# Performance work log

Hardware: AMD Instinct MI355X
Metric: run time of the kernel (lower is better)

The kernel has to match this reference:

```python
import jax, jax.numpy as jnp
import numpy as np

NQ = 4  # n_qubits_per_head


def _apply_ry(state, theta, q):
    # state: (N, 2,2,2,2) real amplitudes; theta: (N,) per-element angle; wire q
    st = jnp.moveaxis(state, 1 + q, -1)
    c = jnp.cos(0.5 * theta).reshape(-1, 1, 1, 1)
    s = jnp.sin(0.5 * theta).reshape(-1, 1, 1, 1)
    a0, a1 = st[..., 0], st[..., 1]
    st = jnp.stack([c * a0 - s * a1, s * a0 + c * a1], axis=-1)
    return jnp.moveaxis(st, -1, 1 + q)


def _apply_cnot(state, ctrl, tgt):
    st = jnp.moveaxis(state, (1 + ctrl, 1 + tgt), (-2, -1))
    st = jnp.stack([st[..., 0, :], st[..., 1, ::-1]], axis=-2)
    return jnp.moveaxis(st, (-2, -1), (1 + ctrl, 1 + tgt))


def _quantum_circuit(x_in, par):
    # x_in: (N, NQ) data angles; par: (N, L, NQ) variational angles (per head, tiled)
    N = x_in.shape[0]
    L = par.shape[1]
    state = jnp.zeros((N, 2, 2, 2, 2), x_in.dtype).at[:, 0, 0, 0, 0].set(1.0)
    for l in range(L):
        for q in range(NQ):
            state = _apply_ry(state, par[:, l, q], q)
        for q in range(NQ - 1):
            state = _apply_cnot(state, q, q + 1)
        state = _apply_cnot(state, NQ - 1, 0)
    for q in range(NQ):
        state = _apply_ry(state, x_in[:, q], q)
    p = state * state  # probabilities (real amplitudes: only RY/CNOT gates)
    zs = []
    for q in range(NQ):
        st = jnp.moveaxis(p, 1 + q, -1)
        zs.append(jnp.sum(st[..., 0], axis=(1, 2, 3)) - jnp.sum(st[..., 1], axis=(1, 2, 3)))
    return jnp.stack(zs, axis=-1)  # (N, NQ)


def setup_inputs() -> dict:
    key = jax.random.key(0)
    ks = jax.random.split(key, 6)
    B, T, E, H, L = 4, 2048, 1024, 16, 2
    scale = 1.0 / np.sqrt(E)
    x = jax.random.normal(ks[0], (B, T, E), dtype=jnp.float32)
    Wq = jax.random.normal(ks[1], (E, E), dtype=jnp.float32) * scale
    Wk = jax.random.normal(ks[2], (E, E), dtype=jnp.float32) * scale
    Wv = jax.random.normal(ks[3], (E, E), dtype=jnp.float32) * scale
    Wo = jax.random.normal(ks[4], (E, E), dtype=jnp.float32) * scale
    qparams = jax.random.normal(ks[5], (H, L, NQ), dtype=jnp.float32)
    return {"x": x, "Wq": Wq, "Wk": Wk, "Wv": Wv, "Wo": Wo, "qparams": qparams}


def reference(x, Wq, Wk, Wv, Wo, qparams):
    B, T, E = x.shape
    H, L, _ = qparams.shape
    hd = E // H
    q = x @ Wq.T
    k = x @ Wk.T
    v = x @ Wv.T
    # NOTE: original scales by sqrt(embed_dim), not sqrt(head_dim)
    scores = jnp.einsum('bte,bse->bts', q, k) / jnp.sqrt(jnp.asarray(E, x.dtype))
    w = jax.nn.softmax(scores, axis=-1)
    out = jnp.einsum('bts,bse->bte', w, v)
    oh = out.reshape(B, T, H, hd)
    N = B * T * H
    xin = oh[..., :NQ].reshape(N, NQ)
    par = jnp.broadcast_to(qparams[None, None], (B, T, H, L, NQ)).reshape(N, L, NQ)
    z = _quantum_circuit(xin, par)  # (N, NQ)
    zfull = jnp.concatenate([z, jnp.zeros((N, hd - NQ), x.dtype)], axis=-1)
    return zfull.reshape(B, T, E) @ Wo.T
```

## Files before the change

### kernel.cpp

```cpp
#include <hip/hip_runtime.h>
#include <hip/hip_fp16.h>

typedef _Float16 half_t;
typedef __attribute__((ext_vector_type(4))) _Float16 half4;
typedef __attribute__((ext_vector_type(8))) _Float16 half8;
typedef __attribute__((ext_vector_type(4))) float floatx4;

__device__ __forceinline__ void async_copy16(const void* src, void* dst_lds) {
  __builtin_amdgcn_global_load_lds(
      (__attribute__((address_space(1))) void*)src,
      (__attribute__((address_space(3))) void*)dst_lds, 16, 0, 0);
}

__global__ __launch_bounds__(512, 2) void gemm_nt_256(
    const half_t* __restrict__ A, const half_t* __restrict__ B,
    half_t* __restrict__ C,
    int lda, int ldb, int ldc, int kIters,
    long sAz2, long sBz2, long sCz2, float scale)
{
  __shared__ __align__(16) half_t sm[2][2][256 * 64];

  const int tid  = threadIdx.x;
  const int wave = tid >> 6, lane = tid & 63;
  const int wm = wave >> 2, wn = wave & 3;
  const int er = lane >> 4, ec = lane & 15;
  const int sw = ec & 7;

  const long z = blockIdx.z;
  const half_t* Ab = A + (long)blockIdx.x * 256 * lda + z * sAz2;
  const half_t* Bb = B + (long)blockIdx.y * 256 * ldb + z * sBz2;

  const int srow = tid >> 3;
  const int skq  = (tid & 7) ^ (srow & 7);

  floatx4 acc[2][2][4][2];
  #pragma unroll
  for (int a = 0; a < 2; a++)
    #pragma unroll
    for (int b = 0; b < 2; b++)
      #pragma unroll
      for (int i = 0; i < 4; i++)
        #pragma unroll
        for (int j = 0; j < 2; j++)
          acc[a][b][i][j] = (floatx4){0.f, 0.f, 0.f, 0.f};

#define STAGE_A(bb, hf, kt) do {                                              \
    const half_t* Ak_ = Ab + (long)(kt) * 64;                                 \
    _Pragma("unroll")                                                         \
    for (int r_ = 0; r_ < 2; r_++) {                                          \
      int lrow_ = r_ * 64 + srow;                                             \
      async_copy16(Ak_ + (long)((hf) * 128 + lrow_) * lda + skq * 8,          \
                   &sm[(bb)][0][(hf) * 8192 + (r_ * 512 + wave * 64) * 8]);   \
    } } while (0)

#define STAGE_B(bb, hf, kt) do {                                              \
    const half_t* Bk_ = Bb + (long)(kt) * 64;                                 \
    _Pragma("unroll")                                                         \
    for (int r_ = 0; r_ < 2; r_++) {                                          \
      int lrow_ = r_ * 64 + srow;                                             \
      async_copy16(Bk_ + (long)((hf) * 128 + lrow_) * ldb + skq * 8,          \
                   &sm[(bb)][1][(hf) * 8192 + (r_ * 512 + wave * 64) * 8]);   \
    } } while (0)

#define DS_A(DST, BB, MH) do {                                                \
    _Pragma("unroll")                                                         \
    for (int ii = 0; ii < 4; ii++) {                                          \
      int row_ = (MH) * 128 + wm * 64 + ii * 16 + ec;                         \
      _Pragma("unroll")                                                       \
      for (int ks = 0; ks < 2; ks++)                                          \
        DST[ii][ks] = *(const half8*)                                         \
            &sm[BB][0][row_ * 64 + (((ks * 4 + er) ^ sw) * 8)];               \
    } } while (0)

#define DS_B(DST, BB, NH) do {                                                \
    _Pragma("unroll")                                                         \
    for (int jj = 0; jj < 2; jj++) {                                          \
      int row_ = (NH) * 128 + wn * 32 + jj * 16 + ec;                         \
      _Pragma("unroll")                                                       \
      for (int ks = 0; ks < 2; ks++)                                          \
        DST[jj][ks] = *(const half8*)                                         \
            &sm[BB][1][row_ * 64 + (((ks * 4 + er) ^ sw) * 8)];               \
    } } while (0)

#define MFMA_Q(AF, BF, MH, NH) do {                                           \
    __builtin_amdgcn_s_setprio(1);                                            \
    _Pragma("unroll")                                                         \
    for (int ks = 0; ks < 2; ks++)                                            \
      _Pragma("unroll")                                                       \
      for (int ii = 0; ii < 4; ii++)                                          \
        _Pragma("unroll")                                                     \
        for (int jj = 0; jj < 2; jj++)                                        \
          acc[MH][NH][ii][jj] = __builtin_amdgcn_mfma_f32_16x16x32_f16(       \
              AF[ii][ks], BF[jj][ks], acc[MH][NH][ii][jj], 0, 0, 0);          \
    __builtin_amdgcn_s_setprio(0);                                            \
  } while (0)

#define BAR() __builtin_amdgcn_s_barrier()
#define LGKM0() do { asm volatile("s_waitcnt lgkmcnt(0)" ::: "memory");       \
                     __builtin_amdgcn_sched_barrier(0); } while (0)
#define VMW(N) asm volatile("s_waitcnt vmcnt(" #N ")" ::: "memory")

  half8 afX[4][2], bfX[2][2], bfY[2][2];
  const int nt = kIters;

  STAGE_A(0, 0, 0); STAGE_B(0, 0, 0); STAGE_B(0, 1, 0); STAGE_A(0, 1, 0);
  STAGE_A(1, 0, 1); STAGE_B(1, 0, 1); STAGE_B(1, 1, 1);
  VMW(6);
  BAR();

  for (int i = 0; i < nt / 2; ++i) {
    const int u = 2 * i, vtl = 2 * i + 1;
    const int nx = (u + 2 < nt);
    DS_A(afX, 0, 0); DS_B(bfX, 0, 0);
    STAGE_A(1, 1, vtl);
    BAR(); LGKM0();
    MFMA_Q(afX, bfX, 0, 0);
    BAR();
    DS_B(bfY, 0, 1);
    if (nx) STAGE_A(0, 0, u + 2);
    BAR(); LGKM0();
    MFMA_Q(afX, bfY, 0, 1);
    BAR();
    DS_A(afX, 0, 1);
    if (nx) STAGE_B(0, 0, u + 2);
    BAR(); LGKM0();
    MFMA_Q(afX, bfY, 1, 1);
    BAR();
    if (nx) STAGE_B(0, 1, u + 2);
    MFMA_Q(afX, bfX, 1, 0);
    if (nx) { VMW(6); } else { VMW(0); }
    BAR();
    DS_A(afX, 1, 0); DS_B(bfX, 1, 0);
    if (nx) STAGE_A(0, 1, u + 2);
    BAR(); LGKM0();
    MFMA_Q(afX, bfX, 0, 0);
    BAR();
    DS_B(bfY, 1, 1);
    if (nx) STAGE_A(1, 0, u + 3);
    BAR(); LGKM0();
    MFMA_Q(afX, bfY, 0, 1);
    BAR();
    DS_A(afX, 1, 1);
    if (nx) STAGE_B(1, 0, u + 3);
    BAR(); LGKM0();
    MFMA_Q(afX, bfY, 1, 1);
    BAR();
    if (nx) STAGE_B(1, 1, u + 3);
    MFMA_Q(afX, bfX, 1, 0);
    if (nx) { VMW(6); } else { VMW(0); }
    BAR();
  }

#undef STAGE_A
#undef STAGE_B
#undef DS_A
#undef DS_B
#undef MFMA_Q
#undef BAR
#undef LGKM0
#undef VMW

  const long rowBase = (long)blockIdx.x * 256;
  const long colBase = (long)blockIdx.y * 256;
  half_t* Cz = C + z * sCz2;
  #pragma unroll
  for (int mh = 0; mh < 2; mh++)
    #pragma unroll
    for (int nh = 0; nh < 2; nh++)
      #pragma unroll
      for (int ii = 0; ii < 4; ii++)
        #pragma unroll
        for (int jj = 0; jj < 2; jj++)
          #pragma unroll
          for (int r = 0; r < 4; r++) {
            long row = rowBase + mh * 128 + wm * 64 + ii * 16 + er * 4 + r;
            long col = colBase + nh * 128 + wn * 32 + jj * 16 + ec;
            Cz[row * (long)ldc + col] =
                (_Float16)(acc[mh][nh][ii][jj][r] * scale);
          }
}

template<int BN, int EPI>
__global__ __launch_bounds__(256) void gemm_nt(
    const half_t* __restrict__ A, const half_t* __restrict__ B,
    void* __restrict__ Cout,
    int lda, int ldb, int ldc, int kIters, int zShift,
    long sAz1, long sBz1, long sCz1,
    long sAz2, long sBz2, long sCz2, float scale,
    const float* __restrict__ qab)
{
  constexpr int BM = 128;
  constexpr int WN = BN / 2;
  constexpr int AN = WN / 16;
  constexpr int RA = BM * 8 / 256;
  constexpr int RB = BN * 8 / 256;
  __shared__ __align__(16) half_t lA[BM * 64];
  __shared__ __align__(16) half_t lB[BN * 64];

  const int tid  = threadIdx.x;
  const int wave = tid >> 6, lane = tid & 63;
  const int wm = wave >> 1, wn = wave & 1;
  const int er = lane >> 4, ec = lane & 15;
  const int sw = ec & 7;

  const long z = blockIdx.z;
  const long z2 = z >> zShift;
  const long z1 = z - (z2 << zShift);
  const half_t* Ab = A + (long)blockIdx.x * BM * lda + z1 * sAz1 + z2 * sAz2;
  const half_t* Bb = B + (long)blockIdx.y * BN * ldb + z1 * sBz1 + z2 * sBz2;
  const long cz = z1 * sCz1 + z2 * sCz2;

  floatx4 acc[4][AN];
  #pragma unroll
  for (int i = 0; i < 4; i++)
    #pragma unroll
    for (int j = 0; j < AN; j++)
      acc[i][j] = (floatx4){0.f, 0.f, 0.f, 0.f};

  for (int ks = 0; ks < kIters; ++ks) {
    const half_t* Ak = Ab + ks * 64;
    const half_t* Bk = Bb + ks * 64;
    #pragma unroll
    for (int r = 0; r < RA; r++) {
      int s = r * 256 + tid;
      int row = s >> 3;
      int kq = (s & 7) ^ (row & 7);
      async_copy16(Ak + (long)row * lda + kq * 8,
                   &lA[(r * 256 + wave * 64) * 8]);
    }
    #pragma unroll
    for (int r = 0; r < RB; r++) {
      int s = r * 256 + tid;
      int row = s >> 3;
      int kq = (s & 7) ^ (row & 7);
      async_copy16(Bk + (long)row * ldb + kq * 8,
                   &lB[(r * 256 + wave * 64) * 8]);
    }
    __syncthreads();

    #pragma unroll
    for (int h = 0; h < 2; h++) {
      half8 af[4], bfv[AN];
      #pragma unroll
      for (int i = 0; i < 4; i++) {
        int row = wm * 64 + i * 16 + ec;
        af[i] = *(const half8*)&lA[row * 64 + (((h * 4 + er) ^ sw) * 8)];
      }
      #pragma unroll
      for (int j = 0; j < AN; j++) {
        int row = wn * WN + j * 16 + ec;
        bfv[j] = *(const half8*)&lB[row * 64 + (((h * 4 + er) ^ sw) * 8)];
      }
      #pragma unroll
      for (int i = 0; i < 4; i++)
        #pragma unroll
        for (int j = 0; j < AN; j++)
          acc[i][j] = __builtin_amdgcn_mfma_f32_16x16x32_f16(
              af[i], bfv[j], acc[i][j], 0, 0, 0);
    }
    __syncthreads();
  }

  const long rowBase = (long)blockIdx.x * BM + wm * 64;
  const long colBase = (long)blockIdx.y * BN + wn * WN;
  #pragma unroll
  for (int i = 0; i < 4; i++)
    #pragma unroll
    for (int j = 0; j < AN; j++)
      #pragma unroll
      for (int r = 0; r < 4; r++) {
        long row = rowBase + i * 16 + er * 4 + r;
        long col = colBase + j * 16 + ec;
        float v = acc[i][j][r];
        if constexpr (EPI == 0) {
          ((half_t*)Cout)[cz + row * (long)ldc + col] = (_Float16)(v * scale);
        } else if constexpr (EPI == 1) {
          ((half_t*)Cout)[cz + col * (long)ldc + row] = (_Float16)v;
        } else if constexpr (EPI == 2) {
          ((float*)Cout)[cz + row * (long)ldc + col] = v * scale;
        } else if constexpr (EPI == 4) {
          ((float*)Cout)[cz + col * (long)ldc + row] = v;
        } else {
          float za = qab[2 * (int)col], zb = qab[2 * (int)col + 1];
          float zv = za * cosf(v) + zb * sinf(v);
          ((half_t*)Cout)[cz + row * (long)ldc + col] = (_Float16)zv;
        }
      }
}

__global__ __launch_bounds__(256) void pv_softmax(
    const half_t* __restrict__ S, const half_t* __restrict__ V,
    float* __restrict__ Op, float* __restrict__ Lp, int kIters)
{
  __shared__ __align__(16) half_t lA[128 * 64];
  __shared__ __align__(16) half_t lB[64 * 64];

  const int tid  = threadIdx.x;
  const int wave = tid >> 6, lane = tid & 63;
  const int wm = wave >> 1, wn = wave & 1;
  const int er = lane >> 4, ec = lane & 15;
  const int sw = ec & 7;

  const long z = blockIdx.z;
  const long z2 = z >> 2;
  const long z1 = z & 3;
  const half_t* Ab = S + (long)blockIdx.x * 128 * 2048
                       + z1 * ((long)2048 * 2048) + z2 * 512;
  const half_t* Bb = V + z1 * 2048 + z2 * 512;

  floatx4 acc[4][2];
  #pragma unroll
  for (int i = 0; i < 4; i++)
    #pragma unroll
    for (int j = 0; j < 2; j++)
      acc[i][j] = (floatx4){0.f, 0.f, 0.f, 0.f};
  float lsum[4] = {0.f, 0.f, 0.f, 0.f};

  for (int ks = 0; ks < kIters; ++ks) {
    const half_t* Ak = Ab + ks * 64;
    const half_t* Bk = Bb + ks * 64;
    #pragma unroll
    for (int r = 0; r < 4; r++) {
      int s = r * 256 + tid;
      int row = s >> 3;
      int kq = (s & 7) ^ (row & 7);
      async_copy16(Ak + (long)row * 2048 + kq * 8,
                   &lA[(r * 256 + wave * 64) * 8]);
    }
    #pragma unroll
    for (int r = 0; r < 2; r++) {
      int s = r * 256 + tid;
      int row = s >> 3;
      int kq = (s & 7) ^ (row & 7);
      async_copy16(Bk + (long)row * 8192 + kq * 8,
                   &lB[(r * 256 + wave * 64) * 8]);
    }
    __syncthreads();

    #pragma unroll
    for (int h = 0; h < 2; h++) {
      half8 af[4], bfv[2];
      #pragma unroll
      for (int i = 0; i < 4; i++) {
        int row = wm * 64 + i * 16 + ec;
        half8 a = *(const half8*)&lA[row * 64 + (((h * 4 + er) ^ sw) * 8)];
        #pragma unroll
        for (int k = 0; k < 8; k++) {
          float e = __expf((float)a[k]);
          _Float16 ph = (_Float16)e;
          a[k] = ph;
          lsum[i] += (float)ph;
        }
        af[i] = a;
      }
      #pragma unroll
      for (int j = 0; j < 2; j++) {
        int row = wn * 32 + j * 16 + ec;
        bfv[j] = *(const half8*)&lB[row * 64 + (((h * 4 + er) ^ sw) * 8)];
      }
      #pragma unroll
      for (int i = 0; i < 4; i++)
        #pragma unroll
        for (int j = 0; j < 2; j++)
          acc[i][j] = __builtin_amdgcn_mfma_f32_16x16x32_f16(
              af[i], bfv[j], acc[i][j], 0, 0, 0);
    }
    __syncthreads();
  }

  const long zo = z2 * ((long)8192 * 64) + z1 * ((long)2048 * 64);
  const long rowBase = (long)blockIdx.x * 128 + wm * 64;
  #pragma unroll
  for (int i = 0; i < 4; i++)
    #pragma unroll
    for (int j = 0; j < 2; j++)
      #pragma unroll
      for (int r = 0; r < 4; r++) {
        long row = rowBase + i * 16 + er * 4 + r;
        long col = wn * 32 + j * 16 + ec;
        Op[zo + row * 64 + col] = acc[i][j][r];
      }

  const long lb = z2 * 8192 + z1 * 2048 + (long)blockIdx.x * 128 + wm * 64;
  #pragma unroll
  for (int i = 0; i < 4; i++) {
    float v = lsum[i];
    v += __shfl_xor(v, 16);
    v += __shfl_xor(v, 32);
    if (wn == 0 && er == 0) Lp[lb + i * 16 + ec] = v;
  }
}

__global__ __launch_bounds__(256) void v4_reduce(const float* __restrict__ P,
                                                 half_t* __restrict__ O)
{
  const long CH = (long)64 * 8192;
  long i = ((long)blockIdx.x * 256 + threadIdx.x) * 4;
  float4 a = *(const float4*)(P + i);
  float4 b = *(const float4*)(P + i + CH);
  float4 c = *(const float4*)(P + i + 2 * CH);
  float4 d = *(const float4*)(P + i + 3 * CH);
  half4 o;
  o[0] = (_Float16)(a.x + b.x + c.x + d.x);
  o[1] = (_Float16)(a.y + b.y + c.y + d.y);
  o[2] = (_Float16)(a.z + b.z + c.z + d.z);
  o[3] = (_Float16)(a.w + b.w + c.w + d.w);
  *(half4*)(O + i) = o;
}

__global__ __launch_bounds__(256) void z_reduce_quantum(
    const float* __restrict__ P, const float* __restrict__ Lp,
    const float* __restrict__ qab, half_t* __restrict__ O)
{
  const long CH = (long)8192 * 64;
  long i = ((long)blockIdx.x * 256 + threadIdx.x) * 4;
  long t = i >> 6;
  float4 a = *(const float4*)(P + i);
  float4 b = *(const float4*)(P + i + CH);
  float4 c = *(const float4*)(P + i + 2 * CH);
  float4 d = *(const float4*)(P + i + 3 * CH);
  float l = Lp[t] + Lp[8192 + t] + Lp[2 * 8192 + t] + Lp[3 * 8192 + t];
  float inv = 1.f / l;
  float s[4] = {(a.x + b.x + c.x + d.x) * inv, (a.y + b.y + c.y + d.y) * inv,
                (a.z + b.z + c.z + d.z) * inv, (a.w + b.w + c.w + d.w) * inv};
  int c0 = (int)(i & 63);
  half4 o;
  #pragma unroll
  for (int j = 0; j < 4; j++) {
    float za = qab[2 * (c0 + j)], zb = qab[2 * (c0 + j) + 1];
    o[j] = (_Float16)(za * cosf(s[j]) + zb * sinf(s[j]));
  }
  *(half4*)(O + i) = o;
}

__global__ __launch_bounds__(256) void softmax_rows(half_t* __restrict__ S,
                                                    int ld)
{
  const long row = blockIdx.x;
  half8* sp = (half8*)(S + row * (long)ld);
  const int t = threadIdx.x;
  const int wave = t >> 6, lane = t & 63;
  half8 hv = sp[t];
  float e[8];
  #pragma unroll
  for (int k = 0; k < 8; k++) e[k] = (float)hv[k];
  float m = e[0];
  #pragma unroll
  for (int k = 1; k < 8; k++) m = fmaxf(m, e[k]);
  #pragma unroll
  for (int o = 32; o > 0; o >>= 1) m = fmaxf(m, __shfl_xor(m, o));
  __shared__ float rmax[4], rsum[4];
  if (lane == 0) rmax[wave] = m;
  __syncthreads();
  m = fmaxf(fmaxf(rmax[0], rmax[1]), fmaxf(rmax[2], rmax[3]));
  float s = 0.f;
  #pragma unroll
  for (int k = 0; k < 8; k++) { e[k] = expf(e[k] - m); s += e[k]; }
  #pragma unroll
  for (int o = 32; o > 0; o >>= 1) s += __shfl_xor(s, o);
  if (lane == 0) rsum[wave] = s;
  __syncthreads();
  float inv = 1.f / (rsum[0] + rsum[1] + rsum[2] + rsum[3]);
  half8 o8;
  #pragma unroll
  for (int k = 0; k < 8; k++) o8[k] = (_Float16)(e[k] * inv);
  sp[t] = o8;
}

__global__ __launch_bounds__(256) void prep_all(
    const float* __restrict__ x,  const float* __restrict__ Wq,
    const float* __restrict__ Wk, const float* __restrict__ Wv,
    const float* __restrict__ Wo, const float* __restrict__ qp, int L,
    half_t* __restrict__ xh, half_t* __restrict__ Wqk,
    half_t* __restrict__ Wv4, half_t* __restrict__ Wos,
    float* __restrict__ qab)
{
  const int bid = blockIdx.x;
  if (bid < 4096) {
    long i = ((long)bid * 256 + threadIdx.x) * 8;
    float4 a = *(const float4*)(x + i);
    float4 b = *(const float4*)(x + i + 4);
    half8 h = {(_Float16)a.x, (_Float16)a.y, (_Float16)a.z, (_Float16)a.w,
               (_Float16)b.x, (_Float16)b.y, (_Float16)b.z, (_Float16)b.w};
    *(half8*)(xh + i) = h;
  } else if (bid < 5120) {
    long i = ((long)(bid - 4096) * 256 + threadIdx.x) * 8;
    int r = (int)(i >> 10);
    int e = (int)(i & 1023);
    const float* src = (r < 1024 ? Wq + (long)r * 1024
                                 : Wk + (long)(r - 1024) * 1024) + e;
    float4 a = *(const float4*)src;
    float4 b = *(const float4*)(src + 4);
    half8 h = {(_Float16)a.x, (_Float16)a.y, (_Float16)a.z, (_Float16)a.w,
               (_Float16)b.x, (_Float16)b.y, (_Float16)b.z, (_Float16)b.w};
    *(half8*)(Wqk + i) = h;
  } else if (bid < 5152) {
    long i = ((long)(bid - 5120) * 256 + threadIdx.x) * 8;
    int c = (int)(i >> 10);
    int e = (int)(i & 1023);
    const float* src = Wv + (long)(((c >> 2) << 6) | (c & 3)) * 1024 + e;
    float4 a = *(const float4*)src;
    float4 b = *(const float4*)(src + 4);
    half8 h = {(_Float16)a.x, (_Float16)a.y, (_Float16)a.z, (_Float16)a.w,
               (_Float16)b.x, (_Float16)b.y, (_Float16)b.z, (_Float16)b.w};
    *(half8*)(Wv4 + i) = h;
  } else if (bid < 5408) {
    int idx = (bid - 5152) * 256 + threadIdx.x;
    int e = idx >> 6, c = idx & 63;
    Wos[idx] = (_Float16)Wo[(long)e * 1024 + (((c >> 2) << 6) | (c & 3))];
  } else {
    int h = threadIdx.x;
    if (h >= 16) return;
    float st[16];
    #pragma unroll
    for (int i = 0; i < 16; i++) st[i] = 0.f;
    st[0] = 1.f;
    for (int l = 0; l < L; l++) {
      #pragma unroll
      for (int q = 0; q < 4; q++) {
        float th = qp[(h * L + l) * 4 + q];
        float c = cosf(0.5f * th), s = sinf(0.5f * th);
        int mq = 8 >> q;
        #pragma unroll
        for (int i = 0; i < 16; i++) {
          if ((i & mq) == 0) {
            float a0 = st[i], a1 = st[i | mq];
            st[i]      = c * a0 - s * a1;
            st[i | mq] = s * a0 + c * a1;
          }
        }
      }
      const int cm[4] = {8, 4, 2, 1};
      const int tm[4] = {4, 2, 1, 8};
      #pragma unroll
      for (int p = 0; p < 4; p++) {
        int mc = cm[p], mt = tm[p];
        #pragma unroll
        for (int i = 0; i < 16; i++) {
          if ((i & mc) != 0 && (i & mt) == 0) {
            float tv = st[i]; st[i] = st[i | mt]; st[i | mt] = tv;
          }
        }
      }
    }
    #pragma unroll
    for (int q = 0; q < 4; q++) {
      int mq = 8 >> q;
      float zc = 0.f, xc = 0.f;
      #pragma unroll
      for (int i = 0; i < 16; i++) {
        float p2 = st[i] * st[i];
        zc += ((i & mq) == 0) ? p2 : -p2;
        if ((i & mq) == 0) xc += st[i] * st[i | mq];
      }
      qab[(h * 4 + q) * 2 + 0] = zc;
      qab[(h * 4 + q) * 2 + 1] = -2.f * xc;
    }
  }
}

extern "C" void kernel_launch(void* const* d_in, const int* in_sizes, int n_in,
                              void* d_out, int out_size, void* d_ws, size_t ws_size,
                              hipStream_t stream)
{
  const float* x  = (const float*)d_in[0];
  const float* Wq = (const float*)d_in[1];
  const float* Wk = (const float*)d_in[2];
  const float* Wv = (const float*)d_in[3];
  const float* Wo = (const float*)d_in[4];
  const float* qp = (const float*)d_in[5];
  const int L = in_sizes[5] / 64;
  float* out = (float*)d_out;

  char* w = (char*)d_ws;
  size_t off = 0;
  auto alloc = [&](size_t bytes) -> void* {
    void* p = w + off;
    off = (off + bytes + 255) & ~(size_t)255;
    return p;
  };
  float*  qab  = (float*)alloc(512);
  half_t* xh   = (half_t*)alloc((size_t)8192 * 1024 * 2);
  half_t* Wqk  = (half_t*)alloc((size_t)2048 * 1024 * 2);
  half_t* Wv4  = (half_t*)alloc((size_t)64 * 1024 * 2);
  half_t* Wos  = (half_t*)alloc((size_t)1024 * 64 * 2);
  half_t* V4th = (half_t*)alloc((size_t)64 * 8192 * 2);
  half_t* Z4   = (half_t*)alloc((size_t)8192 * 64 * 2);
  float*  Lp   = (float*)alloc((size_t)4 * 8192 * 4);

  half_t* QKb = (half_t*)d_out;

  int tier = (ws_size >= off + (size_t)8192 * 2048 * 2 + 256) ? 0 : 1;
  const size_t Sn = (tier == 0) ? (size_t)8192 * 2048 : (size_t)2048 * 2048;
  half_t* S = (half_t*)alloc(Sn * 2);

  prep_all<<<dim3(5409), dim3(256), 0, stream>>>(
      x, Wq, Wk, Wv, Wo, qp, L, xh, Wqk, Wv4, Wos, qab);

  gemm_nt_256<<<dim3(32, 8, 1), 512, 0, stream>>>(
      xh, Wqk, QKb, 1024, 1024, 2048, 16, 0, 0, 0, 1.f);

  if (tier == 0) {
    float* V4p = (float*)S;
    gemm_nt<64, 4><<<dim3(64, 1, 4), 256, 0, stream>>>(
        xh, Wv4, V4p, 1024, 1024, 8192, 4, 0,
        0, 0, 0, 256, 256, (long)64 * 8192, 1.f, nullptr);
    v4_reduce<<<dim3(512), dim3(256), 0, stream>>>(V4p, V4th);

    gemm_nt_256<<<dim3(8, 8, 4), 512, 0, stream>>>(
        QKb, QKb + 1024, S, 2048, 2048, 2048, 16,
        (long)2048 * 2048, (long)2048 * 2048, (long)2048 * 2048, 0.03125f);

    float* Zp = (float*)d_out;
    pv_softmax<<<dim3(16, 1, 16), 256, 0, stream>>>(S, V4th, Zp, Lp, 8);
    z_reduce_quantum<<<dim3(512), dim3(256), 0, stream>>>(Zp, Lp, qab, Z4);
  } else {
    gemm_nt<64, 1><<<dim3(64, 1, 1), 256, 0, stream>>>(
        xh, Wv4, V4th, 1024, 1024, 8192, 16, 0,
        0, 0, 0, 0, 0, 0, 1.f, nullptr);
    for (int b = 0; b < 4; b++) {
      const long q0 = (long)b * 2048;
      gemm_nt<128, 0><<<dim3(16, 16, 1), 256, 0, stream>>>(
          QKb + q0 * 2048, QKb + 1024 + q0 * 2048, S,
          2048, 2048, 2048, 16, 0, 0, 0, 0, 0, 0, 0, 0.03125f, nullptr);
      softmax_rows<<<dim3(2048), dim3(256), 0, stream>>>(S, 2048);
      gemm_nt<64, 5><<<dim3(16, 1, 1), 256, 0, stream>>>(
          S, V4th + q0, Z4 + q0 * 64, 2048, 8192, 64, 32, 0,
          0, 0, 0, 0, 0, 0, 1.f, qab);
    }
  }

  gemm_nt<128, 2><<<dim3(64, 8, 1), 256, 0, stream>>>(
      Z4, Wos, out, 64, 64, 1024, 1, 0,
      0, 0, 0, 0, 0, 0, 1.f, nullptr);
}
```

Baseline: 211.3 us.

## Fuse V4 reduction into QK gemm launch and double PV split-K

Removes the standalone v4_reduce launch by running the reduction in an extra z-slice of blocks in the QK^T gemm kernel, giving V4 partials a dedicated buffer instead of aliasing S. Doubles the split-K factor of the PV/softmax-sum kernel from 4 to 8 chunks to increase block count, with the final reduce summing 8 partials. This cuts launch overhead and improves occupancy, at the cost of more partial-sum traffic and extra workspace.

```diff
diff --git a/kernel.cpp b/kernel.cpp
--- a/kernel.cpp
+++ b/kernel.cpp
@@ -16,8 +16,29 @@
     const half_t* __restrict__ A, const half_t* __restrict__ B,
     half_t* __restrict__ C,
     int lda, int ldb, int ldc, int kIters,
-    long sAz2, long sBz2, long sCz2, float scale)
+    long sAz2, long sBz2, long sCz2, float scale,
+    const float* __restrict__ redP, half_t* __restrict__ redO)
 {
+  if (redP != nullptr && blockIdx.z == 4) {
+    const long CH = (long)64 * 8192;
+    int idx = ((blockIdx.y * 8 + blockIdx.x) << 9) | threadIdx.x;
+    #pragma unroll
+    for (int k = 0; k < 4; k++) {
+      long i = (long)(idx + k * 32768) * 4;
+      float4 a = *(const float4*)(redP + i);
+      float4 b = *(const float4*)(redP + i + CH);
+      float4 c = *(const float4*)(redP + i + 2 * CH);
+      float4 d = *(const float4*)(redP + i + 3 * CH);
+      half4 o;
+      o[0] = (_Float16)(a.x + b.x + c.x + d.x);
+      o[1] = (_Float16)(a.y + b.y + c.y + d.y);
+      o[2] = (_Float16)(a.z + b.z + c.z + d.z);
+      o[3] = (_Float16)(a.w + b.w + c.w + d.w);
+      *(half4*)(redO + i) = o;
+    }
+    return;
+  }
+
   __shared__ __align__(16) half_t sm[2][2][256 * 64];
 
   const int tid  = threadIdx.x;
@@ -305,8 +326,8 @@
   const long z2 = z >> 2;
   const long z1 = z & 3;
   const half_t* Ab = S + (long)blockIdx.x * 128 * 2048
-                       + z1 * ((long)2048 * 2048) + z2 * 512;
-  const half_t* Bb = V + z1 * 2048 + z2 * 512;
+                       + z1 * ((long)2048 * 2048) + z2 * 256;
+  const half_t* Bb = V + z1 * 2048 + z2 * 256;
 
   floatx4 acc[4][2];
   #pragma unroll
@@ -391,23 +412,6 @@
   }
 }
 
-__global__ __launch_bounds__(256) void v4_reduce(const float* __restrict__ P,
-                                                 half_t* __restrict__ O)
-{
-  const long CH = (long)64 * 8192;
-  long i = ((long)blockIdx.x * 256 + threadIdx.x) * 4;
-  float4 a = *(const float4*)(P + i);
-  float4 b = *(const float4*)(P + i + CH);
-  float4 c = *(const float4*)(P + i + 2 * CH);
-  float4 d = *(const float4*)(P + i + 3 * CH);
-  half4 o;
-  o[0] = (_Float16)(a.x + b.x + c.x + d.x);
-  o[1] = (_Float16)(a.y + b.y + c.y + d.y);
-  o[2] = (_Float16)(a.z + b.z + c.z + d.z);
-  o[3] = (_Float16)(a.w + b.w + c.w + d.w);
-  *(half4*)(O + i) = o;
-}
-
 __global__ __launch_bounds__(256) void z_reduce_quantum(
     const float* __restrict__ P, const float* __restrict__ Lp,
     const float* __restrict__ qab, half_t* __restrict__ O)
@@ -415,20 +419,22 @@
   const long CH = (long)8192 * 64;
   long i = ((long)blockIdx.x * 256 + threadIdx.x) * 4;
   long t = i >> 6;
-  float4 a = *(const float4*)(P + i);
-  float4 b = *(const float4*)(P + i + CH);
-  float4 c = *(const float4*)(P + i + 2 * CH);
-  float4 d = *(const float4*)(P + i + 3 * CH);
-  float l = Lp[t] + Lp[8192 + t] + Lp[2 * 8192 + t] + Lp[3 * 8192 + t];
+  float s[4] = {0.f, 0.f, 0.f, 0.f};
+  #pragma unroll
+  for (int c = 0; c < 8; c++) {
+    float4 a = *(const float4*)(P + i + c * CH);
+    s[0] += a.x; s[1] += a.y; s[2] += a.z; s[3] += a.w;
+  }
+  float l = 0.f;
+  #pragma unroll
+  for (int c = 0; c < 8; c++) l += Lp[c * 8192 + t];
   float inv = 1.f / l;
-  float s[4] = {(a.x + b.x + c.x + d.x) * inv, (a.y + b.y + c.y + d.y) * inv,
-                (a.z + b.z + c.z + d.z) * inv, (a.w + b.w + c.w + d.w) * inv};
   int c0 = (int)(i & 63);
   half4 o;
   #pragma unroll
   for (int j = 0; j < 4; j++) {
     float za = qab[2 * (c0 + j)], zb = qab[2 * (c0 + j) + 1];
-    o[j] = (_Float16)(za * cosf(s[j]) + zb * sinf(s[j]));
+    o[j] = (_Float16)(za * cosf(s[j] * inv) + zb * sinf(s[j] * inv));
   }
   *(half4*)(O + i) = o;
 }
@@ -586,7 +592,8 @@
   half_t* Wos  = (half_t*)alloc((size_t)1024 * 64 * 2);
   half_t* V4th = (half_t*)alloc((size_t)64 * 8192 * 2);
   half_t* Z4   = (half_t*)alloc((size_t)8192 * 64 * 2);
-  float*  Lp   = (float*)alloc((size_t)4 * 8192 * 4);
+  float*  Lp   = (float*)alloc((size_t)8 * 8192 * 4);
+  float*  V4p  = (float*)alloc((size_t)4 * 64 * 8192 * 4);
 
   half_t* QKb = (half_t*)d_out;
 
@@ -598,21 +605,20 @@
       x, Wq, Wk, Wv, Wo, qp, L, xh, Wqk, Wv4, Wos, qab);
 
   gemm_nt_256<<<dim3(32, 8, 1), 512, 0, stream>>>(
-      xh, Wqk, QKb, 1024, 1024, 2048, 16, 0, 0, 0, 1.f);
+      xh, Wqk, QKb, 1024, 1024, 2048, 16, 0, 0, 0, 1.f, nullptr, nullptr);
 
   if (tier == 0) {
-    float* V4p = (float*)S;
     gemm_nt<64, 4><<<dim3(64, 1, 4), 256, 0, stream>>>(
         xh, Wv4, V4p, 1024, 1024, 8192, 4, 0,
         0, 0, 0, 256, 256, (long)64 * 8192, 1.f, nullptr);
-    v4_reduce<<<dim3(512), dim3(256), 0, stream>>>(V4p, V4th);
-
-    gemm_nt_256<<<dim3(8, 8, 4), 512, 0, stream>>>(
+
+    gemm_nt_256<<<dim3(8, 8, 5), 512, 0, stream>>>(
         QKb, QKb + 1024, S, 2048, 2048, 2048, 16,
-        (long)2048 * 2048, (long)2048 * 2048, (long)2048 * 2048, 0.03125f);
+        (long)2048 * 2048, (long)2048 * 2048, (long)2048 * 2048, 0.03125f,
+        V4p, V4th);
 
     float* Zp = (float*)d_out;
-    pv_softmax<<<dim3(16, 1, 16), 256, 0, stream>>>(S, V4th, Zp, Lp, 8);
+    pv_softmax<<<dim3(16, 1, 32), 256, 0, stream>>>(S, V4th, Zp, Lp, 4);
     z_reduce_quantum<<<dim3(512), dim3(256), 0, stream>>>(Zp, Lp, qab, Z4);
   } else {
     gemm_nt<64, 1><<<dim3(64, 1, 1), 256, 0, stream>>>(
```

Result: no change. 211.3 us (+0.0%).
